# Kernel tuning notes

Hardware: AMD Instinct MI355X
Metric: run time of the kernel (lower is better)

Reference implementation:

```python
import jax, jax.numpy as jnp
import numpy as np

C = 512
G = 32  # num_norm_groups
EPS = 1e-6


def setup_inputs() -> dict:
    key = jax.random.key(0)
    ks = jax.random.split(key, 10)
    B, H, W = 8, 64, 64
    s = 1.0 / np.sqrt(C)
    return {
        "x": jax.random.normal(ks[0], (B, C, H, W), dtype=jnp.float32),
        "gamma": jnp.ones((C,), jnp.float32),
        "beta": jnp.zeros((C,), jnp.float32),
        "Wq": jax.random.uniform(ks[1], (C, C), jnp.float32, -s, s),
        "bq": jax.random.uniform(ks[2], (C,), jnp.float32, -s, s),
        "Wk": jax.random.uniform(ks[3], (C, C), jnp.float32, -s, s),
        "bk": jax.random.uniform(ks[4], (C,), jnp.float32, -s, s),
        "Wv": jax.random.uniform(ks[5], (C, C), jnp.float32, -s, s),
        "bv": jax.random.uniform(ks[6], (C,), jnp.float32, -s, s),
        "Wo": jax.random.uniform(ks[7], (C, C), jnp.float32, -s, s),
    }


def group_norm(x, gamma, beta):
    # x: [B, C, H, W]; normalize over each group of C//G channels and all spatial dims
    B, Cc, H, W = x.shape
    xg = x.reshape(B, G, Cc // G, H, W)
    mean = jnp.mean(xg, axis=(2, 3, 4), keepdims=True)
    var = jnp.var(xg, axis=(2, 3, 4), keepdims=True)
    xg = (xg - mean) * jax.lax.rsqrt(var + EPS)
    x = xg.reshape(B, Cc, H, W)
    return x * gamma[None, :, None, None] + beta[None, :, None, None]


def reference(x, gamma, beta, Wq, bq, Wk, bk, Wv, bv, Wo):
    B, Cc, H, W = x.shape
    out = group_norm(x, gamma, beta)
    # [B, C, H, W] -> [B, H*W, C]
    out = out.transpose(0, 2, 3, 1).reshape(B, H * W, Cc)
    q = out @ Wq.T + bq
    k = out @ Wk.T + bk
    v = out @ Wv.T + bv
    score = jnp.einsum('bic,bjc->bij', q, k) / jnp.sqrt(jnp.float32(Cc))
    score = jax.nn.softmax(score, axis=-1)
    out = jnp.einsum('bij,bjc->bic', score, v)
    out = out @ Wo.T
    out = out.reshape(B, H, W, Cc).transpose(0, 3, 1, 2)
    return out + x
```

## Files before the change

### kernel.cpp

```cpp
#include <hip/hip_runtime.h>
#include <hip/hip_bf16.h>
#include <cstdint>
#include <cstddef>

typedef __hip_bfloat16 BF;
typedef __attribute__((ext_vector_type(8))) short bhalf8;
typedef __attribute__((ext_vector_type(4))) float floatx4;

#define NB 8
#define NC 512
#define NHW 4096
#define NG 32

__device__ __forceinline__ float b2f(short h) {
    union { unsigned u; float f; } c;
    c.u = ((unsigned)(unsigned short)h) << 16;
    return c.f;
}
__device__ __forceinline__ short f2b(float f) {
    __hip_bfloat16 h = __float2bfloat16(f);
    short s;
    __builtin_memcpy(&s, &h, 2);
    return s;
}

__device__ __forceinline__ void gload16(const BF* g, BF* l) {
    __builtin_amdgcn_global_load_lds(
        (const __attribute__((address_space(1))) void*)g,
        (__attribute__((address_space(3))) void*)l, 16, 0, 0);
}

__device__ __forceinline__ void BARRIER() {
    asm volatile("" ::: "memory");
    __builtin_amdgcn_s_barrier();
    asm volatile("" ::: "memory");
}
#define WAITVM(N) asm volatile("s_waitcnt vmcnt(" #N ")" ::: "memory")
#define WAITLGKM() asm volatile("s_waitcnt lgkmcnt(0)" ::: "memory")

__device__ __forceinline__ void xcd_swizzle(int& bx, int& by) {
    const int gx = gridDim.x;
    const int nwg = gx * gridDim.y;
    if ((nwg & 7) == 0) {
        const int lin = by * gx + bx;
        const int cpx = nwg >> 3;
        const int s = (lin & 7) * cpx + (lin >> 3);
        bx = s % gx;
        by = s / gx;
    }
}

__global__ __launch_bounds__(256) void f2b_convert4(const float* __restrict__ s0,
                                                    const float* __restrict__ s1,
                                                    const float* __restrict__ s2,
                                                    const float* __restrict__ s3,
                                                    BF* __restrict__ dst) {
    const int which = blockIdx.x >> 8;
    const float* src = (which == 0) ? s0 : (which == 1) ? s1 : (which == 2) ? s2 : s3;
    BF* d = dst + (long)which * (NC * NC);
    const int i = ((blockIdx.x & 255) * 256 + threadIdx.x) * 4;
    float4 v = *(const float4*)&src[i];
    d[i]     = __float2bfloat16(v.x);
    d[i + 1] = __float2bfloat16(v.y);
    d[i + 2] = __float2bfloat16(v.z);
    d[i + 3] = __float2bfloat16(v.w);
}

__global__ __launch_bounds__(256) void gn_stats(const float* __restrict__ x,
                                                float* __restrict__ stats) {
    const int bg = blockIdx.x;
    const long base = (long)bg * 65536;
    float s = 0.f, q = 0.f;
    for (int i = threadIdx.x * 4; i < 65536; i += 256 * 4) {
        float4 v4 = *(const float4*)&x[base + i];
        s += v4.x + v4.y + v4.z + v4.w;
        q += v4.x * v4.x + v4.y * v4.y + v4.z * v4.z + v4.w * v4.w;
    }
#pragma unroll
    for (int o = 32; o; o >>= 1) { s += __shfl_down(s, o); q += __shfl_down(q, o); }
    __shared__ float rs[4], rq[4];
    const int w = threadIdx.x >> 6;
    if ((threadIdx.x & 63) == 0) { rs[w] = s; rq[w] = q; }
    __syncthreads();
    if (threadIdx.x == 0) {
        s = rs[0] + rs[1] + rs[2] + rs[3];
        q = rq[0] + rq[1] + rq[2] + rq[3];
        float mean = s * (1.f / 65536.f);
        float var = q * (1.f / 65536.f) - mean * mean;
        stats[2 * bg]     = mean;
        stats[2 * bg + 1] = rsqrtf(fmaxf(var, 0.f) + 1e-6f);
    }
}

__global__ __launch_bounds__(256) void gn_apply(const float* __restrict__ x,
                                                const float* __restrict__ gamma,
                                                const float* __restrict__ beta,
                                                const float* __restrict__ stats,
                                                BF* __restrict__ n) {
    __shared__ float tile[64][65];
    const int b = blockIdx.z, c0 = blockIdx.y * 64, s0 = blockIdx.x * 64;
    const long xbase = ((long)b * NC + c0) * NHW + s0;
#pragma unroll
    for (int i = 0; i < 16; i++) {
        int lin = i * 256 + threadIdx.x;
        int cl = lin >> 6, sl = lin & 63;
        int c = c0 + cl;
        float2 mr = ((const float2*)stats)[b * NG + (c >> 4)];
        float v = x[xbase + (long)cl * NHW + sl];
        v = (v - mr.x) * mr.y * gamma[c] + beta[c];
        tile[cl][sl] = v;
    }
    __syncthreads();
    const long nbase = ((long)b * NHW + s0) * NC + c0;
#pragma unroll
    for (int i = 0; i < 16; i++) {
        int lin = i * 256 + threadIdx.x;
        int sl = lin >> 6, cl = lin & 63;
        n[nbase + (long)sl * NC + cl] = __float2bfloat16(tile[cl][sl]);
    }
}

#define LDA8(buf, mf, ks) (*(const bhalf8*)(sL + (buf) * 65536 + aOff + (mf) * 2048 + (ks) * 64))
#define LDB8(buf, nf, ks) (*(const bhalf8*)(sL + (buf) * 65536 + bOff + (nf) * 2048 + (ks) * 64))
#define QUAD(M0, N0)                                                                     \
    {                                                                                    \
        _Pragma("unroll") for (int mf = (M0); mf < (M0) + 4; mf++)                       \
            _Pragma("unroll") for (int nf = (N0); nf < (N0) + 2; nf++) {                 \
            acc[mf][nf] = __builtin_amdgcn_mfma_f32_16x16x32_bf16(                       \
                aR[mf & 3][0], bR[nf][0], acc[mf][nf], 0, 0, 0);                         \
            acc[mf][nf] = __builtin_amdgcn_mfma_f32_16x16x32_bf16(                       \
                aR[mf & 3][1], bR[nf][1], acc[mf][nf], 0, 0, 0);                         \
        }                                                                                \
    }

template <bool BIAS, bool TRANS, bool RESID>
__global__ __launch_bounds__(512) void gemm256(
    const BF* __restrict__ A, long aStride,
    const BF* __restrict__ Bm, long bStride,
    BF* __restrict__ C, long cStride,
    const float* __restrict__ bias,
    const float* __restrict__ resid, float* __restrict__ outF,
    int M, int N, int K, float scale)
{
    __shared__ __align__(16) char sL[131072];
    const int tid = threadIdx.x;
    const int wave = tid >> 6, lane = tid & 63;
    int bxi = blockIdx.x, byi = blockIdx.y;
    xcd_swizzle(bxi, byi);
    const int bm = byi * 256, bn = bxi * 256;
    const BF* Ab = A + (long)blockIdx.z * aStride + (long)bm * K;
    const BF* Bb = Bm + (long)blockIdx.z * bStride + (long)bn * K;

    const int d0 = tid * 16, d1 = 8192 + tid * 16;
    const int p0 = d0 ^ (((d0 >> 9) & 1) << 5);
    const int p1 = d1 ^ (((d1 >> 9) & 1) << 5);
    const int soff0 = (p0 >> 7) * K + ((p0 & 127) >> 1);
    const int soff1 = (p1 >> 7) * K + ((p1 & 127) >> 1);
    const int lds0 = wave * 1024;
    const int lds1 = 8192 + wave * 1024;

    const int lr = lane & 15, lk2 = (lane >> 4) * 16;
    const int sbase = (lr * 128 + lk2) ^ (((lr >> 2) & 1) << 5);
    const int aOff = (wave >> 2) * 16384 + sbase;
    const int bOff = (2 + ((wave >> 1) & 1)) * 16384 + (wave & 1) * 8192 + sbase;

    auto STAGE = [&](int t, int region, int dbuf) {
        const BF* g = ((region < 2) ? (Ab + (long)region * 128 * K)
                                    : (Bb + (long)(region - 2) * 128 * K)) + (long)t * 64;
        char* lb = sL + dbuf * 65536 + region * 16384;
        gload16(g + soff0, (BF*)(lb + lds0));
        gload16(g + soff1, (BF*)(lb + lds1));
    };

    floatx4 acc[8][4];
#pragma unroll
    for (int i = 0; i < 8; i++)
#pragma unroll
        for (int j = 0; j < 4; j++) acc[i][j] = (floatx4){0.f, 0.f, 0.f, 0.f};

    const int nt = K >> 6, ngrp = nt >> 1;

    STAGE(0, 0, 0); STAGE(0, 1, 0); STAGE(0, 2, 0); STAGE(0, 3, 0);
    WAITVM(4);
    STAGE(1, 2, 1); STAGE(1, 3, 1); STAGE(1, 0, 1);
    WAITVM(6);
    BARRIER();

    bhalf8 aR[4][2], bR[4][2];

    for (int g = 0; g < ngrp; ++g) {
        const bool st = (g < ngrp - 1);
        const int t2 = 2 * g + 2, t3 = 2 * g + 3;

#pragma unroll
        for (int mf = 0; mf < 4; mf++) { aR[mf][0] = LDA8(0, mf, 0); aR[mf][1] = LDA8(0, mf, 1); }
#pragma unroll
        for (int nf = 0; nf < 2; nf++) { bR[nf][0] = LDB8(0, nf, 0); bR[nf][1] = LDB8(0, nf, 1); }
        if (!(wave & 2)) {
#pragma unroll
            for (int nf = 2; nf < 4; nf++) { bR[nf][0] = LDB8(0, nf, 0); bR[nf][1] = LDB8(0, nf, 1); }
        }
        STAGE(2 * g + 1, 1, 1);
        BARRIER(); WAITLGKM();
        __builtin_amdgcn_s_setprio(1);
        QUAD(0, 0);
        __builtin_amdgcn_s_setprio(0);
        BARRIER();

        if (wave & 2) {
#pragma unroll
            for (int nf = 2; nf < 4; nf++) { bR[nf][0] = LDB8(0, nf, 0); bR[nf][1] = LDB8(0, nf, 1); }
        }
        if (st) STAGE(t2, 2, 0);
        BARRIER(); WAITLGKM();
        __builtin_amdgcn_s_setprio(1);
        QUAD(0, 2);
        __builtin_amdgcn_s_setprio(0);
        BARRIER();

#pragma unroll
        for (int mf = 4; mf < 8; mf++) { aR[mf & 3][0] = LDA8(0, mf, 0); aR[mf & 3][1] = LDA8(0, mf, 1); }
        if (st) STAGE(t2, 3, 0);
        BARRIER(); WAITLGKM();
        __builtin_amdgcn_s_setprio(1);
        QUAD(4, 0);
        __builtin_amdgcn_s_setprio(0);
        BARRIER();

        if (st) STAGE(t2, 0, 0);
        BARRIER();
        __builtin_amdgcn_s_setprio(1);
        QUAD(4, 2);
        __builtin_amdgcn_s_setprio(0);
        if (st) { WAITVM(6); } else { WAITVM(0); }
        BARRIER();

#pragma unroll
        for (int mf = 0; mf < 4; mf++) { aR[mf][0] = LDA8(1, mf, 0); aR[mf][1] = LDA8(1, mf, 1); }
#pragma unroll
        for (int nf = 0; nf < 2; nf++) { bR[nf][0] = LDB8(1, nf, 0); bR[nf][1] = LDB8(1, nf, 1); }
        if (!(wave & 2)) {
#pragma unroll
            for (int nf = 2; nf < 4; nf++) { bR[nf][0] = LDB8(1, nf, 0); bR[nf][1] = LDB8(1, nf, 1); }
        }
        if (st) STAGE(t2, 1, 0);
        BARRIER(); WAITLGKM();
        __builtin_amdgcn_s_setprio(1);
        QUAD(0, 0);
        __builtin_amdgcn_s_setprio(0);
        BARRIER();

        if (wave & 2) {
#pragma unroll
            for (int nf = 2; nf < 4; nf++) { bR[nf][0] = LDB8(1, nf, 0); bR[nf][1] = LDB8(1, nf, 1); }
        }
        if (st) STAGE(t3, 2, 1);
        BARRIER(); WAITLGKM();
        __builtin_amdgcn_s_setprio(1);
        QUAD(0, 2);
        __builtin_amdgcn_s_setprio(0);
        BARRIER();

#pragma unroll
        for (int mf = 4; mf < 8; mf++) { aR[mf & 3][0] = LDA8(1, mf, 0); aR[mf & 3][1] = LDA8(1, mf, 1); }
        if (st) STAGE(t3, 3, 1);
        BARRIER(); WAITLGKM();
        __builtin_amdgcn_s_setprio(1);
        QUAD(4, 0);
        __builtin_amdgcn_s_setprio(0);
        BARRIER();

        if (st) STAGE(t3, 0, 1);
        BARRIER();
        __builtin_amdgcn_s_setprio(1);
        QUAD(4, 2);
        __builtin_amdgcn_s_setprio(0);
        if (st) { WAITVM(6); }
        BARRIER();
    }

    const int wm = (wave >> 2) * 128, wn = (wave & 3) * 64;
    if (RESID) {
        float* Ob = outF + (long)blockIdx.z * cStride;
        const float* Xb = resid + (long)blockIdx.z * cStride;
#pragma unroll
        for (int nf = 0; nf < 4; nf++) {
            const int col = bn + wn + nf * 16 + lr;
#pragma unroll
            for (int mf = 0; mf < 8; mf++) {
                const int row0 = bm + wm + mf * 16 + (lane >> 4) * 4;
                const long a = (long)col * M + row0;
                float4 xv = *(const float4*)&Xb[a];
                float4 ov;
                ov.x = acc[mf][nf][0] * scale + xv.x;
                ov.y = acc[mf][nf][1] * scale + xv.y;
                ov.z = acc[mf][nf][2] * scale + xv.z;
                ov.w = acc[mf][nf][3] * scale + xv.w;
                *(float4*)&Ob[a] = ov;
            }
        }
        return;
    }
    BF* Cb = C + (long)blockIdx.z * cStride;
#pragma unroll
    for (int nf = 0; nf < 4; nf++) {
        const int col = bn + wn + nf * 16 + lr;
        const float bv = BIAS ? bias[col] : 0.0f;
#pragma unroll
        for (int mf = 0; mf < 8; mf++) {
            const int row0 = bm + wm + mf * 16 + (lane >> 4) * 4;
#pragma unroll
            for (int r = 0; r < 4; r++) {
                float v = acc[mf][nf][r] * scale + bv;
                if (TRANS) Cb[(long)col * M + row0 + r] = __float2bfloat16(v);
                else       Cb[(long)(row0 + r) * N + col] = __float2bfloat16(v);
            }
        }
    }
}

template <bool BIAS, bool TRANS>
__global__ __launch_bounds__(256, 2) void gemm128(
    const BF* __restrict__ A, long aStride,
    const BF* __restrict__ Bm, long bStride,
    BF* __restrict__ C, long cStride,
    const float* __restrict__ bias,
    int M, int N, int K, float scale)
{
    __shared__ __align__(16) BF sA[128 * 32];
    __shared__ __align__(16) BF sB[128 * 32];
    const int tid = threadIdx.x;
    const int wave = tid >> 6, lane = tid & 63;
    int bxi = blockIdx.x, byi = blockIdx.y;
    xcd_swizzle(bxi, byi);
    const int bm = byi * 128, bn = bxi * 128;
    const BF* Ab = A + (long)blockIdx.z * aStride + (long)bm * K;
    const BF* Bb = Bm + (long)blockIdx.z * bStride + (long)bn * K;

    const int srow = wave * 32 + (lane >> 2);
    const int sk = (lane & 3) * 8;
    const BF* gA0 = Ab + (long)srow * K + sk;
    const BF* gA1 = gA0 + (long)16 * K;
    const BF* gB0 = Bb + (long)srow * K + sk;
    const BF* gB1 = gB0 + (long)16 * K;
    BF* lA0 = &sA[(wave * 32) * 32];
    BF* lA1 = &sA[(wave * 32 + 16) * 32];
    BF* lB0 = &sB[(wave * 32) * 32];
    BF* lB1 = &sB[(wave * 32 + 16) * 32];

    floatx4 acc[4][4];
#pragma unroll
    for (int i = 0; i < 4; i++)
#pragma unroll
        for (int j = 0; j < 4; j++) acc[i][j] = (floatx4){0.f, 0.f, 0.f, 0.f};

    const int wm = (wave >> 1) * 64, wn = (wave & 1) * 64;
    const int lr = lane & 15, lk = (lane >> 4) * 8;

    for (int k0 = 0; k0 < K; k0 += 32) {
        __syncthreads();
        gload16(gA0 + k0, lA0);
        gload16(gA1 + k0, lA1);
        gload16(gB0 + k0, lB0);
        gload16(gB1 + k0, lB1);
        __syncthreads();
        bhalf8 af[4], bfr[4];
#pragma unroll
        for (int i = 0; i < 4; i++)
            af[i] = *(const bhalf8*)&sA[(wm + i * 16 + lr) * 32 + lk];
#pragma unroll
        for (int i = 0; i < 4; i++)
            bfr[i] = *(const bhalf8*)&sB[(wn + i * 16 + lr) * 32 + lk];
#pragma unroll
        for (int mi = 0; mi < 4; mi++)
#pragma unroll
            for (int ni = 0; ni < 4; ni++)
                acc[mi][ni] = __builtin_amdgcn_mfma_f32_16x16x32_bf16(
                    af[mi], bfr[ni], acc[mi][ni], 0, 0, 0);
    }

    BF* Cb = C + (long)blockIdx.z * cStride;
#pragma unroll
    for (int ni = 0; ni < 4; ni++) {
        const int col = bn + wn + ni * 16 + lr;
        const float bv = BIAS ? bias[col] : 0.0f;
#pragma unroll
        for (int mi = 0; mi < 4; mi++) {
            const int row0 = bm + wm + mi * 16 + (lane >> 4) * 4;
#pragma unroll
            for (int r = 0; r < 4; r++) {
                float v = acc[mi][ni][r] * scale + bv;
                if (TRANS) Cb[(long)col * M + row0 + r] = __float2bfloat16(v);
                else       Cb[(long)(row0 + r) * N + col] = __float2bfloat16(v);
            }
        }
    }
}

__global__ __launch_bounds__(256, 2) void gemm64(
    const BF* __restrict__ A, long aStride,
    const BF* __restrict__ Bm, long bStride,
    BF* __restrict__ C, long cStride,
    int N, int K, float scale)
{
    __shared__ __align__(16) BF sA[64 * 32];
    __shared__ __align__(16) BF sB[128 * 32];
    const int tid = threadIdx.x;
    const int wave = tid >> 6, lane = tid & 63;
    int bxi = blockIdx.x, byi = blockIdx.y;
    xcd_swizzle(bxi, byi);
    const int bm = byi * 64, bn = bxi * 128;
    const BF* Ab = A + (long)blockIdx.z * aStride + (long)bm * K;
    const BF* Bb = Bm + (long)blockIdx.z * bStride + (long)bn * K;

    const int rowoff = lane >> 2, sk = (lane & 3) * 8;
    const BF* gA0 = Ab + (long)(wave * 16 + rowoff) * K + sk;
    const BF* gB0 = Bb + (long)(wave * 32 + rowoff) * K + sk;
    const BF* gB1 = gB0 + (long)16 * K;
    BF* lA0 = &sA[(wave * 16) * 32];
    BF* lB0 = &sB[(wave * 32) * 32];
    BF* lB1 = &sB[(wave * 32 + 16) * 32];

    floatx4 acc[2][4];
#pragma unroll
    for (int i = 0; i < 2; i++)
#pragma unroll
        for (int j = 0; j < 4; j++) acc[i][j] = (floatx4){0.f, 0.f, 0.f, 0.f};

    const int wm = (wave >> 1) * 32, wn = (wave & 1) * 64;
    const int lr = lane & 15, lk = (lane >> 4) * 8;

    for (int k0 = 0; k0 < K; k0 += 32) {
        __syncthreads();
        gload16(gA0 + k0, lA0);
        gload16(gB0 + k0, lB0);
        gload16(gB1 + k0, lB1);
        __syncthreads();
        bhalf8 af[2], bfr[4];
#pragma unroll
        for (int i = 0; i < 2; i++)
            af[i] = *(const bhalf8*)&sA[(wm + i * 16 + lr) * 32 + lk];
#pragma unroll
        for (int i = 0; i < 4; i++)
            bfr[i] = *(const bhalf8*)&sB[(wn + i * 16 + lr) * 32 + lk];
#pragma unroll
        for (int mi = 0; mi < 2; mi++)
#pragma unroll
            for (int ni = 0; ni < 4; ni++)
                acc[mi][ni] = __builtin_amdgcn_mfma_f32_16x16x32_bf16(
                    af[mi], bfr[ni], acc[mi][ni], 0, 0, 0);
    }

    BF* Cb = C + (long)blockIdx.z * cStride;
#pragma unroll
    for (int ni = 0; ni < 4; ni++) {
        const int col = bn + wn + ni * 16 + lr;
#pragma unroll
        for (int mi = 0; mi < 2; mi++) {
            const int row0 = bm + wm + mi * 16 + (lane >> 4) * 4;
#pragma unroll
            for (int r = 0; r < 4; r++)
                Cb[(long)(row0 + r) * N + col] = __float2bfloat16(acc[mi][ni][r] * scale);
        }
    }
}

__global__ __launch_bounds__(256) void softmax4096(BF* __restrict__ S) {
    const long base = (long)blockIdx.x * 4096 + threadIdx.x * 16;
    const int tid = threadIdx.x, w = tid >> 6;
    bhalf8 u = *(bhalf8*)&S[base];
    bhalf8 u2 = *(bhalf8*)&S[base + 8];
    float v[16];
    float m = -1e30f;
#pragma unroll
    for (int j = 0; j < 8; j++) { v[j] = b2f(u[j]); v[8 + j] = b2f(u2[j]); }
#pragma unroll
    for (int j = 0; j < 16; j++) m = fmaxf(m, v[j]);
#pragma unroll
    for (int o = 32; o; o >>= 1) m = fmaxf(m, __shfl_xor(m, o));
    __shared__ float rm[4], rs[4];
    if ((tid & 63) == 0) rm[w] = m;
    __syncthreads();
    m = fmaxf(fmaxf(rm[0], rm[1]), fmaxf(rm[2], rm[3]));
    float s = 0.f;
#pragma unroll
    for (int j = 0; j < 16; j++) { v[j] = __expf(v[j] - m); s += v[j]; }
#pragma unroll
    for (int o = 32; o; o >>= 1) s += __shfl_xor(s, o);
    if ((tid & 63) == 0) rs[w] = s;
    __syncthreads();
    s = rs[0] + rs[1] + rs[2] + rs[3];
    const float inv = 1.0f / s;
#pragma unroll
    for (int j = 0; j < 8; j++) { u[j] = f2b(v[j] * inv); u2[j] = f2b(v[8 + j] * inv); }
    *(bhalf8*)&S[base] = u;
    *(bhalf8*)&S[base + 8] = u2;
}

extern "C" void kernel_launch(void* const* d_in, const int* in_sizes, int n_in,
                              void* d_out, int out_size, void* d_ws, size_t ws_size,
                              hipStream_t stream) {
    const float* x     = (const float*)d_in[0];
    const float* gamma = (const float*)d_in[1];
    const float* beta  = (const float*)d_in[2];
    const float* Wq    = (const float*)d_in[3];
    const float* bq    = (const float*)d_in[4];
    const float* Wk    = (const float*)d_in[5];
    const float* bk    = (const float*)d_in[6];
    const float* Wv    = (const float*)d_in[7];
    const float* bv    = (const float*)d_in[8];
    const float* Wo    = (const float*)d_in[9];
    float* out = (float*)d_out;

    const long ACTB = (long)NHW * NC;
    const long SB   = (long)NHW * NHW;
    const long WSZ  = (long)NC * NC;

    char* ws = (char*)d_ws;
    float* stats = (float*)ws;
    BF* wb = (BF*)(ws + 4096);
    BF* q  = wb + 4 * WSZ;
    BF* kk = q + NB * ACTB;
    BF* vT = kk + NB * ACTB;
    BF* R  = vT + NB * ACTB;
    BF* n = R;
    BF* S = R;

    const size_t base_need = 4096ull + (size_t)4 * WSZ * 2 + (size_t)3 * NB * ACTB * 2;
    long sroom = (ws_size > base_need) ? (long)((ws_size - base_need) / (SB * 2)) : 1;
    int chunk = (int)(sroom < 1 ? 1 : (sroom > NB ? NB : sroom));
    while (NB % chunk) chunk--;

    f2b_convert4<<<1024, 256, 0, stream>>>(Wq, Wk, Wv, Wo, wb);

    gn_stats<<<NB * NG, 256, 0, stream>>>(x, stats);
    gn_apply<<<dim3(NHW / 64, NC / 64, NB), 256, 0, stream>>>(x, gamma, beta, stats, n);

    gemm256<true, false, false><<<dim3(NC / 256, NHW / 256, NB), 512, 0, stream>>>(
        n, ACTB, wb + 0 * WSZ, 0, q, ACTB, bq, nullptr, nullptr, NHW, NC, NC, 1.0f);
    gemm256<true, false, false><<<dim3(NC / 256, NHW / 256, NB), 512, 0, stream>>>(
        n, ACTB, wb + 1 * WSZ, 0, kk, ACTB, bk, nullptr, nullptr, NHW, NC, NC, 1.0f);
    gemm256<true, true, false><<<dim3(NC / 256, NHW / 256, NB), 512, 0, stream>>>(
        n, ACTB, wb + 2 * WSZ, 0, vT, ACTB, bv, nullptr, nullptr, NHW, NC, NC, 1.0f);

    const float iscl = 0.044194173824159216f;
    for (int b0 = 0; b0 < NB; b0 += chunk) {
        gemm256<false, false, false><<<dim3(NHW / 256, NHW / 256, chunk), 512, 0, stream>>>(
            q + b0 * ACTB, ACTB, kk + b0 * ACTB, ACTB, S, SB, nullptr, nullptr, nullptr,
            NHW, NHW, NC, iscl);
        softmax4096<<<NHW * chunk, 256, 0, stream>>>(S);
        if (chunk >= 4)
            gemm256<false, false, false><<<dim3(NC / 256, NHW / 256, chunk), 512, 0, stream>>>(
                S, SB, vT + b0 * ACTB, ACTB, q + b0 * ACTB, ACTB, nullptr, nullptr, nullptr,
                NHW, NC, NHW, 1.0f);
        else if (chunk == 2)
            gemm128<false, false><<<dim3(NC / 128, NHW / 128, chunk), 256, 0, stream>>>(
                S, SB, vT + b0 * ACTB, ACTB, q + b0 * ACTB, ACTB, nullptr, NHW, NC, NHW, 1.0f);
        else
            gemm64<<<dim3(NC / 128, NHW / 64, chunk), 256, 0, stream>>>(
                S, SB, vT + b0 * ACTB, ACTB, q + b0 * ACTB, ACTB, NC, NHW, 1.0f);
    }

    gemm256<false, true, true><<<dim3(NC / 256, NHW / 256, NB), 512, 0, stream>>>(
        q, ACTB, wb + 3 * WSZ, 0, nullptr, ACTB, nullptr, x, out, NHW, NC, NC, 1.0f);
}
```

Before: 825.1 us.

## Split-K the attention-times-V GEMM and widen the LDS swizzle

Adds a split-K variant of the 256x256 GEMM for the score-times-V product. It doubles the grid by splitting K=4096 into two halves that write fp32 partials, followed by a reduce kernel that sums them and converts to bf16. This targets the low block count of that GEMM (only 2x16xchunk tiles) and the resulting poor CU occupancy. It also changes the LDS XOR swizzle to an 8-row pattern and adds explicit lda/ldb strides. The cost is extra fp32 partial traffic, an extra launch, and more workspace, and the path is enabled only when the workspace is large enough.

```diff
diff --git a/kernel.cpp b/kernel.cpp
--- a/kernel.cpp
+++ b/kernel.cpp
@@ -120,8 +120,8 @@
     }
 }
 
-#define LDA8(buf, mf, ks) (*(const bhalf8*)(sL + (buf) * 65536 + aOff + (mf) * 2048 + (ks) * 64))
-#define LDB8(buf, nf, ks) (*(const bhalf8*)(sL + (buf) * 65536 + bOff + (nf) * 2048 + (ks) * 64))
+#define LDA8(buf, mf, ks) (*(const bhalf8*)(sL + (buf) * 65536 + ((ks) ? aOff1 : aOff0) + (mf) * 2048))
+#define LDB8(buf, nf, ks) (*(const bhalf8*)(sL + (buf) * 65536 + ((ks) ? bOff1 : bOff0) + (nf) * 2048))
 #define QUAD(M0, N0)                                                                     \
     {                                                                                    \
         _Pragma("unroll") for (int mf = (M0); mf < (M0) + 4; mf++)                       \
@@ -133,14 +133,14 @@
         }                                                                                \
     }
 
-template <bool BIAS, bool TRANS, bool RESID>
+template <bool BIAS, bool TRANS, bool RESID, bool SPLITK>
 __global__ __launch_bounds__(512) void gemm256(
     const BF* __restrict__ A, long aStride,
     const BF* __restrict__ Bm, long bStride,
     BF* __restrict__ C, long cStride,
     const float* __restrict__ bias,
     const float* __restrict__ resid, float* __restrict__ outF,
-    int M, int N, int K, float scale)
+    int M, int N, int K, float scale, long lda, long ldb)
 {
     __shared__ __align__(16) char sL[131072];
     const int tid = threadIdx.x;
@@ -148,28 +148,38 @@
     int bxi = blockIdx.x, byi = blockIdx.y;
     xcd_swizzle(bxi, byi);
     const int bm = byi * 256, bn = bxi * 256;
-    const BF* Ab = A + (long)blockIdx.z * aStride + (long)bm * K;
-    const BF* Bb = Bm + (long)blockIdx.z * bStride + (long)bn * K;
+    const int zz = blockIdx.z;
+    const int bz = SPLITK ? (zz >> 1) : zz;
+    const int kh = SPLITK ? (zz & 1) : 0;
+    const BF* Ab = A + (long)bz * aStride + (long)kh * K + (long)bm * lda;
+    const BF* Bb = Bm + (long)bz * bStride + (long)kh * K + (long)bn * ldb;
 
     const int d0 = tid * 16, d1 = 8192 + tid * 16;
-    const int p0 = d0 ^ (((d0 >> 9) & 1) << 5);
-    const int p1 = d1 ^ (((d1 >> 9) & 1) << 5);
-    const int soff0 = (p0 >> 7) * K + ((p0 & 127) >> 1);
-    const int soff1 = (p1 >> 7) * K + ((p1 & 127) >> 1);
+    const int r0 = d0 >> 7, r1 = d1 >> 7;
+    const int c0s = ((d0 ^ ((r0 & 7) << 4)) & 127) >> 1;
+    const int c1s = ((d1 ^ ((r1 & 7) << 4)) & 127) >> 1;
+    const long sA0 = (long)r0 * lda + c0s, sA1 = (long)r1 * lda + c1s;
+    const long sB0 = (long)r0 * ldb + c0s, sB1 = (long)r1 * ldb + c1s;
     const int lds0 = wave * 1024;
     const int lds1 = 8192 + wave * 1024;
 
     const int lr = lane & 15, lk2 = (lane >> 4) * 16;
-    const int sbase = (lr * 128 + lk2) ^ (((lr >> 2) & 1) << 5);
-    const int aOff = (wave >> 2) * 16384 + sbase;
-    const int bOff = (2 + ((wave >> 1) & 1)) * 16384 + (wave & 1) * 8192 + sbase;
+    const int swz = (lr & 7) << 4;
+    const int sb0 = lr * 128 + (lk2 ^ swz);
+    const int sb1 = lr * 128 + ((lk2 + 64) ^ swz);
+    const int aReg = (wave >> 2) * 16384;
+    const int bReg = (2 + ((wave >> 1) & 1)) * 16384 + (wave & 1) * 8192;
+    const int aOff0 = aReg + sb0, aOff1 = aReg + sb1;
+    const int bOff0 = bReg + sb0, bOff1 = bReg + sb1;
 
     auto STAGE = [&](int t, int region, int dbuf) {
-        const BF* g = ((region < 2) ? (Ab + (long)region * 128 * K)
-                                    : (Bb + (long)(region - 2) * 128 * K)) + (long)t * 64;
+        const bool isA = region < 2;
+        const long ld = isA ? lda : ldb;
+        const BF* g = (isA ? (Ab + (long)region * 128 * ld)
+                           : (Bb + (long)(region - 2) * 128 * ld)) + (long)t * 64;
         char* lb = sL + dbuf * 65536 + region * 16384;
-        gload16(g + soff0, (BF*)(lb + lds0));
-        gload16(g + soff1, (BF*)(lb + lds1));
+        gload16(g + (isA ? sA0 : sB0), (BF*)(lb + lds0));
+        gload16(g + (isA ? sA1 : sB1), (BF*)(lb + lds1));
     };
 
     floatx4 acc[8][4];
@@ -280,9 +290,24 @@
     }
 
     const int wm = (wave >> 2) * 128, wn = (wave & 3) * 64;
+    if (SPLITK) {
+        float* Ob = outF + (long)zz * cStride;
+#pragma unroll
+        for (int nf = 0; nf < 4; nf++) {
+            const int col = bn + wn + nf * 16 + lr;
+#pragma unroll
+            for (int mf = 0; mf < 8; mf++) {
+                const int row0 = bm + wm + mf * 16 + (lane >> 4) * 4;
+#pragma unroll
+                for (int r = 0; r < 4; r++)
+                    Ob[(long)(row0 + r) * N + col] = acc[mf][nf][r] * scale;
+            }
+        }
+        return;
+    }
     if (RESID) {
-        float* Ob = outF + (long)blockIdx.z * cStride;
-        const float* Xb = resid + (long)blockIdx.z * cStride;
+        float* Ob = outF + (long)zz * cStride;
+        const float* Xb = resid + (long)zz * cStride;
 #pragma unroll
         for (int nf = 0; nf < 4; nf++) {
             const int col = bn + wn + nf * 16 + lr;
@@ -301,7 +326,7 @@
         }
         return;
     }
-    BF* Cb = C + (long)blockIdx.z * cStride;
+    BF* Cb = C + (long)zz * cStride;
 #pragma unroll
     for (int nf = 0; nf < 4; nf++) {
         const int col = bn + wn + nf * 16 + lr;
@@ -317,6 +342,22 @@
             }
         }
     }
+}
+
+__global__ __launch_bounds__(256) void splitk_reduce(const float* __restrict__ P,
+                                                     BF* __restrict__ dst,
+                                                     long perBatch) {
+    const long off = ((long)blockIdx.x * 256 + threadIdx.x) * 4;
+    const float* p0 = P + (long)blockIdx.y * 2 * perBatch;
+    float4 a = *(const float4*)&p0[off];
+    float4 b = *(const float4*)&p0[perBatch + off];
+    BF* d = dst + (long)blockIdx.y * perBatch + off;
+    short4 o;
+    o.x = f2b(a.x + b.x);
+    o.y = f2b(a.y + b.y);
+    o.z = f2b(a.z + b.z);
+    o.w = f2b(a.w + b.w);
+    *(short4*)d = o;
 }
 
 template <bool BIAS, bool TRANS>
@@ -531,36 +572,48 @@
     int chunk = (int)(sroom < 1 ? 1 : (sroom > NB ? NB : sroom));
     while (NB % chunk) chunk--;
 
+    float* Pf = (float*)(R + (long)chunk * SB);
+    const size_t splitNeed = base_need + (size_t)chunk * SB * 2
+                           + (size_t)chunk * 2 * ACTB * 4;
+    const bool doSplit = (chunk >= 2) && (ws_size >= splitNeed);
+
     f2b_convert4<<<1024, 256, 0, stream>>>(Wq, Wk, Wv, Wo, wb);
 
     gn_stats<<<NB * NG, 256, 0, stream>>>(x, stats);
     gn_apply<<<dim3(NHW / 64, NC / 64, NB), 256, 0, stream>>>(x, gamma, beta, stats, n);
 
-    gemm256<true, false, false><<<dim3(NC / 256, NHW / 256, NB), 512, 0, stream>>>(
-        n, ACTB, wb + 0 * WSZ, 0, q, ACTB, bq, nullptr, nullptr, NHW, NC, NC, 1.0f);
-    gemm256<true, false, false><<<dim3(NC / 256, NHW / 256, NB), 512, 0, stream>>>(
-        n, ACTB, wb + 1 * WSZ, 0, kk, ACTB, bk, nullptr, nullptr, NHW, NC, NC, 1.0f);
-    gemm256<true, true, false><<<dim3(NC / 256, NHW / 256, NB), 512, 0, stream>>>(
-        n, ACTB, wb + 2 * WSZ, 0, vT, ACTB, bv, nullptr, nullptr, NHW, NC, NC, 1.0f);
+    gemm256<true, false, false, false><<<dim3(NC / 256, NHW / 256, NB), 512, 0, stream>>>(
+        n, ACTB, wb + 0 * WSZ, 0, q, ACTB, bq, nullptr, nullptr, NHW, NC, NC, 1.0f, NC, NC);
+    gemm256<true, false, false, false><<<dim3(NC / 256, NHW / 256, NB), 512, 0, stream>>>(
+        n, ACTB, wb + 1 * WSZ, 0, kk, ACTB, bk, nullptr, nullptr, NHW, NC, NC, 1.0f, NC, NC);
+    gemm256<true, true, false, false><<<dim3(NC / 256, NHW / 256, NB), 512, 0, stream>>>(
+        n, ACTB, wb + 2 * WSZ, 0, vT, ACTB, bv, nullptr, nullptr, NHW, NC, NC, 1.0f, NC, NC);
 
     const float iscl = 0.044194173824159216f;
     for (int b0 = 0; b0 < NB; b0 += chunk) {
-        gemm256<false, false, false><<<dim3(NHW / 256, NHW / 256, chunk), 512, 0, stream>>>(
+        gemm256<false, false, false, false><<<dim3(NHW / 256, NHW / 256, chunk), 512, 0, stream>>>(
             q + b0 * ACTB, ACTB, kk + b0 * ACTB, ACTB, S, SB, nullptr, nullptr, nullptr,
-            NHW, NHW, NC, iscl);
+            NHW, NHW, NC, iscl, NC, NC);
         softmax4096<<<NHW * chunk, 256, 0, stream>>>(S);
-        if (chunk >= 4)
-            gemm256<false, false, false><<<dim3(NC / 256, NHW / 256, chunk), 512, 0, stream>>>(
+        if (doSplit) {
+            gemm256<false, false, false, true><<<dim3(NC / 256, NHW / 256, chunk * 2), 512, 0, stream>>>(
+                S, SB, vT + b0 * ACTB, ACTB, nullptr, ACTB, nullptr, nullptr, Pf,
+                NHW, NC, NHW / 2, 1.0f, NHW, NHW);
+            splitk_reduce<<<dim3((unsigned)(ACTB / 1024), chunk), 256, 0, stream>>>(
+                Pf, q + b0 * ACTB, ACTB);
+        } else if (chunk >= 4) {
+            gemm256<false, false, false, false><<<dim3(NC / 256, NHW / 256, chunk), 512, 0, stream>>>(
                 S, SB, vT + b0 * ACTB, ACTB, q + b0 * ACTB, ACTB, nullptr, nullptr, nullptr,
-                NHW, NC, NHW, 1.0f);
-        else if (chunk == 2)
+                NHW, NC, NHW, 1.0f, NHW, NHW);
+        } else if (chunk == 2) {
             gemm128<false, false><<<dim3(NC / 128, NHW / 128, chunk), 256, 0, stream>>>(
                 S, SB, vT + b0 * ACTB, ACTB, q + b0 * ACTB, ACTB, nullptr, NHW, NC, NHW, 1.0f);
-        else
+        } else {
             gemm64<<<dim3(NC / 128, NHW / 64, chunk), 256, 0, stream>>>(
                 S, SB, vT + b0 * ACTB, ACTB, q + b0 * ACTB, ACTB, NC, NHW, 1.0f);
-    }
-
-    gemm256<false, true, true><<<dim3(NC / 256, NHW / 256, NB), 512, 0, stream>>>(
-        q, ACTB, wb + 3 * WSZ, 0, nullptr, ACTB, nullptr, x, out, NHW, NC, NC, 1.0f);
-}
+        }
+    }
+
+    gemm256<false, true, true, false><<<dim3(NC / 256, NHW / 256, NB), 512, 0, stream>>>(
+        q, ACTB, wb + 3 * WSZ, 0, nullptr, ACTB, nullptr, x, out, NHW, NC, NC, 1.0f, NC, NC);
+}
```

Result: faster. 790.9 us (-4.1%).
